# Optimization experiments

Hardware: AMD Instinct MI355X
Metric: run time of the kernel (lower is better)

Reference implementation:

```python
import jax, jax.numpy as jnp
import numpy as np

B, S, IN, H, Q, M, K = 32, 2048, 128, 256, 16, 64, 3


def setup_inputs() -> dict:
    key = jax.random.key(0)
    ks = jax.random.split(key, 12)
    rn = lambda k, shp, s=0.05: (jax.random.normal(k, shp, jnp.float32) * s)
    return {
        "input_sequence": rn(ks[0], (B, S, IN), 1.0),
        "W_ih0": rn(ks[1], (4 * H, IN)),
        "W_hh0": rn(ks[2], (4 * H, H)),
        "b_ih0": jnp.zeros((4 * H,), jnp.float32),
        "b_hh0": jnp.zeros((4 * H,), jnp.float32),
        "W_ih1": rn(ks[3], (4 * H, H)),
        "W_hh1": rn(ks[4], (4 * H, H)),
        "b_ih1": jnp.zeros((4 * H,), jnp.float32),
        "b_hh1": jnp.zeros((4 * H,), jnp.float32),
        "W_cq": rn(ks[5], (Q, H)),
        "b_cq": jnp.zeros((Q,), jnp.float32),
        "mem_keys": rn(ks[6], (M, Q), 1.0),
        "mem_vals": rn(ks[7], (M, H), 1.0),
        "W_out": rn(ks[8], (H, 2 * H)),
        "b_out": jnp.zeros((H,), jnp.float32),
        "classical_weight": jnp.float32(0.7),
        "quantum_weight": jnp.float32(0.3),
    }


def _lstm_layer(x, W_ih, W_hh, b_ih, b_hh):
    """PyTorch-convention LSTM layer (gate order i,f,g,o), batch_first input."""
    Bb = x.shape[0]
    Hh = W_hh.shape[1]
    # precompute the input contribution for all timesteps: [B,S,4H]
    xg = jnp.einsum('bsi,gi->bsg', x, W_ih) + b_ih + b_hh

    def step(carry, xt):
        h, c = carry
        g = xt + h @ W_hh.T  # [B,4H]
        i, f, gg, o = jnp.split(g, 4, axis=-1)
        i = jax.nn.sigmoid(i)
        f = jax.nn.sigmoid(f)
        gg = jnp.tanh(gg)
        o = jax.nn.sigmoid(o)
        c = f * c + i * gg
        h = o * jnp.tanh(c)
        return (h, c), h

    init = (jnp.zeros((Bb, Hh), x.dtype), jnp.zeros((Bb, Hh), x.dtype))
    _, hs = jax.lax.scan(step, init, jnp.swapaxes(xg, 0, 1))  # [S,B,H]
    return jnp.swapaxes(hs, 0, 1)


def _forward(input_sequence, W_ih0, W_hh0, b_ih0, b_hh0, W_ih1, W_hh1, b_ih1,
             b_hh1, W_cq, b_cq, mem_keys, mem_vals, W_out, b_out,
             classical_weight, quantum_weight):
    # classical 2-layer LSTM
    h1 = _lstm_layer(input_sequence, W_ih0, W_hh0, b_ih0, b_hh0)
    lstm_out = _lstm_layer(h1, W_ih1, W_hh1, b_ih1, b_hh1)  # [B,S,H]

    # classical_to_quantum + tanh -> per-token query [B,S,Q]
    q = jnp.tanh(jnp.einsum('bsh,qh->bsq', lstm_out, W_cq) + b_cq)

    # batched k-NN read over the quantum memory (cosine similarity, k=3)
    eps = jnp.float32(1e-8)
    qn = q / (jnp.linalg.norm(q, axis=-1, keepdims=True) + eps)
    kn = mem_keys / (jnp.linalg.norm(mem_keys, axis=-1, keepdims=True) + eps)
    sims = jnp.einsum('bsq,mq->bsm', qn, kn)          # [B,S,M]
    top_vals, top_idx = jax.lax.top_k(sims, K)        # [B,S,K]
    gathered = mem_vals[top_idx]                      # [B,S,K,H]

    # similarity-weighted average of retrieved contents
    tot = jnp.sum(top_vals, axis=-1, keepdims=True)   # [B,S,1]
    weighted = jnp.einsum('bsk,bskh->bsh', top_vals, gathered)
    enhanced = jnp.where(tot > 0, weighted / jnp.where(tot == 0, 1.0, tot), 0.0)

    # combine streams and project
    combined = jnp.concatenate(
        [classical_weight * lstm_out, quantum_weight * enhanced], axis=-1)
    out = jnp.einsum('bsc,hc->bsh', combined, W_out) + b_out  # [B,S,H]
    return out


def reference(input_sequence, W_ih0, W_hh0, b_ih0, b_hh0, W_ih1, W_hh1, b_ih1,
              b_hh1, W_cq, b_cq, mem_keys, mem_vals, W_out, b_out,
              classical_weight, quantum_weight):
    return _forward(input_sequence, W_ih0, W_hh0, b_ih0, b_hh0, W_ih1, W_hh1,
                    b_ih1, b_hh1, W_cq, b_cq, mem_keys, mem_vals, W_out, b_out,
                    classical_weight, quantum_weight)
```

## Files before the change

kernel.cpp:

```cpp
#include <hip/hip_runtime.h>
#include <cstdint>
#include <cstddef>
#include <math.h>

#define B_   32
#define S_   2048
#define IN_  128
#define H_   256
#define Q_   16
#define M_   64
#define D_   4

__device__ __forceinline__ float4 ld4(const float* p) { return *(const float4*)p; }

#define AGLD(p)    __hip_atomic_load((p),  __ATOMIC_RELAXED, __HIP_MEMORY_SCOPE_AGENT)
#define AGST(p, v) __hip_atomic_store((p), (v), __ATOMIC_RELAXED, __HIP_MEMORY_SCOPE_AGENT)

__global__ __launch_bounds__(256, 1) void lstm2(
    const float* __restrict__ x,
    const float* __restrict__ Wih0, const float* __restrict__ bih0,
    const float* __restrict__ bhh0, const float* __restrict__ Whh0,
    const float* __restrict__ Wih1, const float* __restrict__ bih1,
    const float* __restrict__ bhh1, const float* __restrict__ Whh1,
    float* __restrict__ out,
    unsigned int* __restrict__ ex)
{
  const int f = blockIdx.x;
  const int n = (f >> 3) & 7;
  const int b = (f >> 6) * 8 + (f & 7);

  const int tid  = threadIdx.x;
  const int w    = tid >> 6;
  const int l    = tid & 63;
  const int cl   = l >> 1;
  const int half = l & 1;

  __shared__ float wih1_lds[128 * 257];
  __shared__ float aring[8][256];
  __shared__ float h_sh[256];
  __shared__ float x_sh[2][IN_];
  __shared__ float g0_sh[4][32], g1_sh[4][32];

#pragma unroll
  for (int s2 = 0; s2 < 8; s2++) aring[s2][tid] = 0.0f;
  h_sh[tid] = 0.0f;

  const int grow = w * 256 + n * 32 + cl;

  float4 wf0[32], wf1[32], wi0[16];
  {
    const float* p0  = Whh0 + (size_t)grow * 256 + half * 128;
    const float* p1  = Whh1 + (size_t)grow * 256 + half * 128;
    const float* pi0 = Wih0 + (size_t)grow * IN_ + half * 64;
#pragma unroll
    for (int i = 0; i < 32; i++) { wf0[i] = ld4(p0 + 4 * i); wf1[i] = ld4(p1 + 4 * i); }
#pragma unroll
    for (int i = 0; i < 16; i++) wi0[i] = ld4(pi0 + 4 * i);
  }
  {
    const int r = tid >> 1, hs = tid & 1;
    const int growR = (r >> 5) * 256 + n * 32 + (r & 31);
    const float* src = Wih1 + (size_t)growR * 256 + hs * 128;
    float* dst = wih1_lds + r * 257 + hs * 128;
#pragma unroll
    for (int i = 0; i < 32; i++) *(float4*)(dst + 4 * i) = ld4(src + 4 * i);
  }
  const float rb0 = (half == 0) ? (bih0[grow] + bhh0[grow]) : 0.0f;
  const float rb1 = (half == 0) ? (bih1[grow] + bhh1[grow]) : 0.0f;
  const float* wih1_row = wih1_lds + (w * 32 + cl) * 257 + half * 128;

  const float* xrow = x + (size_t)b * S_ * IN_;
  float* outp = out + (size_t)b * S_ * H_;
  unsigned int* exb = ex + (size_t)b * 2048;

  if (tid < IN_) {
    x_sh[0][tid] = xrow[tid];
    x_sh[1][tid] = xrow[IN_ + tid];
  }
  float xreg = (tid < IN_) ? xrow[(size_t)2 * IN_ + tid] : 0.0f;
  float c0 = 0.0f, c1 = 0.0f;
  float xa1 = 0.0f;
  __syncthreads();

  float xa0;
  {
    const float* xb = &x_sh[0][half * 64];
    float4 s = {0, 0, 0, 0};
#pragma unroll
    for (int i = 0; i < 16; i++) {
      float4 v = *(const float4*)(xb + 4 * i);
      s.x += wi0[i].x * v.x; s.y += wi0[i].y * v.y;
      s.z += wi0[i].z * v.z; s.w += wi0[i].w * v.w;
    }
    xa0 = (s.x + s.y) + (s.z + s.w) + rb0;
  }

  bool dead = false;
  for (int t = 0; t < S_ + D_; ++t) {
    const bool doA = (t < S_);
    const int  u   = t - D_;
    const bool doH = (u >= 0);

    float g0 = 0.0f, g1 = 0.0f;
    if (doA) {
      const float* ap = &aring[(t - 1) & 7][half * 128];
      float4 s = {0, 0, 0, 0};
#pragma unroll
      for (int i = 0; i < 32; i++) {
        float4 v = *(const float4*)(ap + 4 * i);
        s.x += wf0[i].x * v.x; s.y += wf0[i].y * v.y;
        s.z += wf0[i].z * v.z; s.w += wf0[i].w * v.w;
      }
      g0 = (s.x + s.y) + (s.z + s.w) + xa0;
      g0 += __shfl_xor(g0, 1);
    }
    if (doH) {
      const float* hp = &h_sh[half * 128];
      float4 s = {0, 0, 0, 0};
#pragma unroll
      for (int i = 0; i < 32; i++) {
        float4 v = *(const float4*)(hp + 4 * i);
        s.x += wf1[i].x * v.x; s.y += wf1[i].y * v.y;
        s.z += wf1[i].z * v.z; s.w += wf1[i].w * v.w;
      }
      g1 = (s.x + s.y) + (s.z + s.w) + xa1;
      g1 += __shfl_xor(g1, 1);
    }
    if (half == 0) {
      if (doA) g0_sh[w][cl] = g0;
      if (doH) g1_sh[w][cl] = g1;
    }
    __syncthreads();

    if (tid < 32 && doA) {
      float gi = g0_sh[0][tid], gf = g0_sh[1][tid];
      float gg = g0_sh[2][tid], go = g0_sh[3][tid];
      float ig = 1.0f / (1.0f + expf(-gi));
      float fg = 1.0f / (1.0f + expf(-gf));
      float cg = tanhf(gg);
      float og = 1.0f / (1.0f + expf(-go));
      c0 = fg * c0 + ig * cg;
      float a = og * tanhf(c0);
      unsigned bits = __float_as_uint(a);
      unsigned tag  = (unsigned)(t + 1) << 16;
      const int p = t & 1, e = n * 32 + tid;
      AGST(exb + (((0 * 2 + p) * 2 + 0) << 8) + e, tag | (bits >> 16));
      AGST(exb + (((0 * 2 + p) * 2 + 1) << 8) + e, tag | (bits & 0xffffu));
    } else if (tid >= 64 && tid < 96 && doH) {
      const int j = tid - 64;
      float gi = g1_sh[0][j], gf = g1_sh[1][j];
      float gg = g1_sh[2][j], go = g1_sh[3][j];
      float ig = 1.0f / (1.0f + expf(-gi));
      float fg = 1.0f / (1.0f + expf(-gf));
      float cg = tanhf(gg);
      float og = 1.0f / (1.0f + expf(-go));
      c1 = fg * c1 + ig * cg;
      float h = og * tanhf(c1);
      outp[(size_t)u * H_ + n * 32 + j] = h;
      unsigned bits = __float_as_uint(h);
      unsigned tag  = (unsigned)(u + 1) << 16;
      const int p = u & 1, e = n * 32 + j;
      AGST(exb + (((1 * 2 + p) * 2 + 0) << 8) + e, tag | (bits >> 16));
      AGST(exb + (((1 * 2 + p) * 2 + 1) << 8) + e, tag | (bits & 0xffffu));
    }

    if (t + 1 < S_) {
      const float* xb = &x_sh[(t + 1) & 1][half * 64];
      float4 s = {0, 0, 0, 0};
#pragma unroll
      for (int i = 0; i < 16; i++) {
        float4 v = *(const float4*)(xb + 4 * i);
        s.x += wi0[i].x * v.x; s.y += wi0[i].y * v.y;
        s.z += wi0[i].z * v.z; s.w += wi0[i].w * v.w;
      }
      xa0 = (s.x + s.y) + (s.z + s.w) + rb0;
    }
    {
      const int v = t - D_ + 1;
      if (v >= 0 && v < S_) {
        const float* av = &aring[v & 7][half * 128];
        float4 s = {0, 0, 0, 0};
#pragma unroll
        for (int i = 0; i < 32; i++) {
          float4 wv = *(const float4*)(wih1_row + 4 * i);
          float4 a4 = *(const float4*)(av + 4 * i);
          s.x += wv.x * a4.x; s.y += wv.y * a4.y;
          s.z += wv.z * a4.z; s.w += wv.w * a4.w;
        }
        xa1 = (s.x + s.y) + (s.z + s.w) + rb1;
      }
    }
    float xreg_n = 0.0f;
    if (tid < IN_ && t + 2 < S_) {
      int tn = (t + 3 < S_) ? t + 3 : S_ - 1;
      xreg_n = xrow[(size_t)tn * IN_ + tid];
    }

    if (!dead && (doA || doH)) {
      const unsigned eA = (unsigned)(t + 1) & 0xffffu;
      const unsigned eH = (unsigned)(u + 1) & 0xffffu;
      const int pa = t & 1, ph = u & 1;
      unsigned int* aHi = exb + (((0 * 2 + pa) * 2 + 0) << 8) + tid;
      unsigned int* aLo = exb + (((0 * 2 + pa) * 2 + 1) << 8) + tid;
      unsigned int* hHi = exb + (((1 * 2 + ph) * 2 + 0) << 8) + tid;
      unsigned int* hLo = exb + (((1 * 2 + ph) * 2 + 1) << 8) + tid;
      unsigned a0v = 0, a1v = 0, h0v = 0, h1v = 0;
      bool needA = doA, needH = doH;
      unsigned guard = 0;
      while (true) {
        if (needA) {
          a0v = AGLD(aHi); a1v = AGLD(aLo);
          if ((a0v >> 16) == eA && (a1v >> 16) == eA) needA = false;
        }
        if (needH) {
          h0v = AGLD(hHi); h1v = AGLD(hLo);
          if ((h0v >> 16) == eH && (h1v >> 16) == eH) needH = false;
        }
        if (!needA && !needH) break;
        if (++guard >= (1u << 20)) { dead = true; break; }
      }
      if (doA) aring[t & 7][tid] = __uint_as_float((a0v << 16) | (a1v & 0xffffu));
      if (doH) h_sh[tid]         = __uint_as_float((h0v << 16) | (h1v & 0xffffu));
    }
    if (tid < IN_ && t < S_) x_sh[t & 1][tid] = xreg;
    xreg = xreg_n;
    __syncthreads();
  }
}

__global__ __launch_bounds__(256) void knn_enh(
    const float* __restrict__ lstm, const float* __restrict__ Wcq,
    const float* __restrict__ bcq, const float* __restrict__ keys,
    const float* __restrict__ vals, const float* __restrict__ qwp,
    float* __restrict__ enh)
{
  const int tid  = threadIdx.x;
  const int wave = tid >> 6, lane = tid & 63;
  const int t = blockIdx.x * 4 + wave;

  __shared__ float xsh[4][256];
  __shared__ float qsh[4][16];

  const float* xrow = lstm + (size_t)t * H_;
  float4 x4 = ld4(xrow + lane * 4);
  *(float4*)&xsh[wave][lane * 4] = x4;
  __syncthreads();

  const int j = lane & 15, seg = lane >> 4;
  const float* wrow = Wcq + j * H_ + seg * 64;
  const float* xseg = &xsh[wave][seg * 64];
  float p = 0.0f;
#pragma unroll
  for (int c = 0; c < 64; c += 4) {
    float4 w4 = ld4(wrow + c);
    p += w4.x * xseg[c] + w4.y * xseg[c + 1] + w4.z * xseg[c + 2] + w4.w * xseg[c + 3];
  }
  p += __shfl_xor(p, 16);
  p += __shfl_xor(p, 32);
  float q = tanhf(p + bcq[j]);

  float sq = q * q;
  sq += __shfl_xor(sq, 1); sq += __shfl_xor(sq, 2);
  sq += __shfl_xor(sq, 4); sq += __shfl_xor(sq, 8);
  float qn = q / (sqrtf(sq) + 1e-8f);
  if (lane < 16) qsh[wave][lane] = qn;
  __syncthreads();

  const int m = lane;
  const float* krow = keys + m * Q_;
  float kv[16]; float kn2 = 0.0f;
#pragma unroll
  for (int jj = 0; jj < 16; jj++) { kv[jj] = krow[jj]; kn2 += kv[jj] * kv[jj]; }
  float rn = 1.0f / (sqrtf(kn2) + 1e-8f);
  float sim = 0.0f;
#pragma unroll
  for (int jj = 0; jj < 16; jj++) sim += qsh[wave][jj] * kv[jj];
  sim *= rn;

  float rem = sim;
  float tv[3]; int ti[3];
#pragma unroll
  for (int k = 0; k < 3; k++) {
    float v = rem; int idx = m;
#pragma unroll
    for (int d = 1; d < 64; d <<= 1) {
      float ov = __shfl_xor(v, d);
      int   oi = __shfl_xor(idx, d);
      if (ov > v || (ov == v && oi < idx)) { v = ov; idx = oi; }
    }
    tv[k] = v; ti[k] = idx;
    if (m == idx) rem = -INFINITY;
  }
  float tot = tv[0] + tv[1] + tv[2];

  float ex = 0, ey = 0, ez = 0, ew = 0;
#pragma unroll
  for (int k = 0; k < 3; k++) {
    float4 vv = ld4(vals + (size_t)ti[k] * H_ + lane * 4);
    ex += tv[k] * vv.x; ey += tv[k] * vv.y;
    ez += tv[k] * vv.z; ew += tv[k] * vv.w;
  }
  float inv = (tot > 0.0f) ? 1.0f / tot : 0.0f;
  const float qw = qwp[0];

  float4 o;
  o.x = qw * ex * inv; o.y = qw * ey * inv;
  o.z = qw * ez * inv; o.w = qw * ew * inv;
  *(float4*)&enh[(size_t)t * H_ + lane * 4] = o;
}

__global__ __launch_bounds__(256) void gemm_cat(
    float* __restrict__ io, const float* __restrict__ A2,
    const float* __restrict__ Bw, const float* __restrict__ bias,
    const float* __restrict__ cwp)
{
  __shared__ float As[16][68];
  __shared__ float Bs[16][260];
  const int tid  = threadIdx.x;
  const int row0 = blockIdx.x * 64;
  const int tx = tid & 15, ty = tid >> 4;
  const int lr = tid >> 2;
  const int lk = (tid & 3) << 2;
  const float cw = cwp[0];

  float acc[4][16];
#pragma unroll
  for (int i = 0; i < 4; i++)
#pragma unroll
    for (int j = 0; j < 16; j++) acc[i][j] = 0.0f;

  for (int k0 = 0; k0 < 512; k0 += 16) {
    float4 av;
    if (k0 < 256) {
      av = ld4(io + (size_t)(row0 + lr) * 256 + k0 + lk);
      av.x *= cw; av.y *= cw; av.z *= cw; av.w *= cw;
    } else {
      av = ld4(A2 + (size_t)(row0 + lr) * 256 + (k0 - 256) + lk);
    }
    As[lk + 0][lr] = av.x; As[lk + 1][lr] = av.y;
    As[lk + 2][lr] = av.z; As[lk + 3][lr] = av.w;
    const float* bp = Bw + (size_t)tid * 512 + k0;
#pragma unroll
    for (int q = 0; q < 4; q++) {
      float4 b4 = ld4(bp + 4 * q);
      Bs[4 * q + 0][tid] = b4.x; Bs[4 * q + 1][tid] = b4.y;
      Bs[4 * q + 2][tid] = b4.z; Bs[4 * q + 3][tid] = b4.w;
    }
    __syncthreads();
#pragma unroll
    for (int k = 0; k < 16; k++) {
      float4 a4 = *(const float4*)&As[k][ty << 2];
      float aa[4] = {a4.x, a4.y, a4.z, a4.w};
#pragma unroll
      for (int cc = 0; cc < 4; cc++) {
        float4 b4 = *(const float4*)&Bs[k][cc * 64 + (tx << 2)];
        float bb[4] = {b4.x, b4.y, b4.z, b4.w};
#pragma unroll
        for (int i = 0; i < 4; i++)
#pragma unroll
          for (int jj = 0; jj < 4; jj++) acc[i][cc * 4 + jj] += aa[i] * bb[jj];
      }
    }
    __syncthreads();
  }

#pragma unroll
  for (int i = 0; i < 4; i++) {
#pragma unroll
    for (int cc = 0; cc < 4; cc++) {
      int c0 = cc * 64 + (tx << 2);
      float4 o;
      o.x = acc[i][cc * 4 + 0] + bias[c0 + 0];
      o.y = acc[i][cc * 4 + 1] + bias[c0 + 1];
      o.z = acc[i][cc * 4 + 2] + bias[c0 + 2];
      o.w = acc[i][cc * 4 + 3] + bias[c0 + 3];
      *(float4*)&io[(size_t)(row0 + (ty << 2) + i) * 256 + c0] = o;
    }
  }
}

extern "C" void kernel_launch(void* const* d_in, const int* in_sizes, int n_in,
                              void* d_out, int out_size, void* d_ws, size_t ws_size,
                              hipStream_t stream)
{
  const float* x    = (const float*)d_in[0];
  const float* Wih0 = (const float*)d_in[1];
  const float* Whh0 = (const float*)d_in[2];
  const float* bih0 = (const float*)d_in[3];
  const float* bhh0 = (const float*)d_in[4];
  const float* Wih1 = (const float*)d_in[5];
  const float* Whh1 = (const float*)d_in[6];
  const float* bih1 = (const float*)d_in[7];
  const float* bhh1 = (const float*)d_in[8];
  const float* Wcq  = (const float*)d_in[9];
  const float* bcq  = (const float*)d_in[10];
  const float* keys = (const float*)d_in[11];
  const float* vals = (const float*)d_in[12];
  const float* Wout = (const float*)d_in[13];
  const float* bout = (const float*)d_in[14];
  const float* cw   = (const float*)d_in[15];
  const float* qw   = (const float*)d_in[16];
  float* out = (float*)d_out;

  const size_t HE = (size_t)B_ * S_ * H_;
  if (ws_size < HE * sizeof(float)) return;
  unsigned int* ex = (unsigned int*)d_ws;
  float* enh = (float*)d_ws;

  const int MT = B_ * S_;
  dim3 blk(256);

  hipMemsetAsync(ex, 0, (size_t)32 * 2048 * sizeof(unsigned int), stream);
  lstm2<<<dim3(256), blk, 0, stream>>>(x, Wih0, bih0, bhh0, Whh0,
                                       Wih1, bih1, bhh1, Whh1, out, ex);

  knn_enh<<<dim3(MT / 4), blk, 0, stream>>>(out, Wcq, bcq, keys, vals, qw, enh);

  gemm_cat<<<dim3(MT / 64), blk, 0, stream>>>(out, enh, Wout, bout, cw);
}
```

Baseline: 15.51 ms.

## Compute all four gates per column group to remove intra-step barrier

Restructures the per-step work mapping so that each group of 8 lanes owns one hidden column and computes all four gate dot products, reducing them with xor shuffles. The gate nonlinearities and cell update are then done redundantly in every lane of the group, which eliminates the shared-memory gate staging and the mid-step __syncthreads. The hidden-state buffer becomes a double-buffered ring so the single remaining barrier is enough. The trade-off is more shuffle reductions and redundant transcendental work, plus a different LDS access pattern for the weights and activations.

```diff
diff --git a/kernel.cpp b/kernel.cpp
--- a/kernel.cpp
+++ b/kernel.cpp
@@ -29,45 +29,46 @@
   const int n = (f >> 3) & 7;
   const int b = (f >> 6) * 8 + (f & 7);
 
-  const int tid  = threadIdx.x;
-  const int w    = tid >> 6;
-  const int l    = tid & 63;
-  const int cl   = l >> 1;
-  const int half = l & 1;
-
-  __shared__ float wih1_lds[128 * 257];
+  const int tid = threadIdx.x;
+  const int w   = tid >> 6;
+  const int l   = tid & 63;
+  const int kc  = l & 7;
+  const int rg  = l >> 3;
+  const int wrg = w * 8 + rg;
+  const int col = n * 32 + wrg;
+
+  __shared__ float w1[128][257];
   __shared__ float aring[8][256];
-  __shared__ float h_sh[256];
+  __shared__ float hring[2][256];
   __shared__ float x_sh[2][IN_];
-  __shared__ float g0_sh[4][32], g1_sh[4][32];
 
 #pragma unroll
   for (int s2 = 0; s2 < 8; s2++) aring[s2][tid] = 0.0f;
-  h_sh[tid] = 0.0f;
-
-  const int grow = w * 256 + n * 32 + cl;
-
-  float4 wf0[32], wf1[32], wi0[16];
-  {
-    const float* p0  = Whh0 + (size_t)grow * 256 + half * 128;
-    const float* p1  = Whh1 + (size_t)grow * 256 + half * 128;
-    const float* pi0 = Wih0 + (size_t)grow * IN_ + half * 64;
-#pragma unroll
-    for (int i = 0; i < 32; i++) { wf0[i] = ld4(p0 + 4 * i); wf1[i] = ld4(p1 + 4 * i); }
-#pragma unroll
-    for (int i = 0; i < 16; i++) wi0[i] = ld4(pi0 + 4 * i);
-  }
-  {
-    const int r = tid >> 1, hs = tid & 1;
-    const int growR = (r >> 5) * 256 + n * 32 + (r & 31);
-    const float* src = Wih1 + (size_t)growR * 256 + hs * 128;
-    float* dst = wih1_lds + r * 257 + hs * 128;
-#pragma unroll
-    for (int i = 0; i < 32; i++) *(float4*)(dst + 4 * i) = ld4(src + 4 * i);
-  }
-  const float rb0 = (half == 0) ? (bih0[grow] + bhh0[grow]) : 0.0f;
-  const float rb1 = (half == 0) ? (bih1[grow] + bhh1[grow]) : 0.0f;
-  const float* wih1_row = wih1_lds + (w * 32 + cl) * 257 + half * 128;
+  hring[0][tid] = 0.0f;
+  hring[1][tid] = 0.0f;
+
+  float4 wf0[4][8], wf1[4][8], wi0[4][4];
+  float rb0[4], rb1[4];
+#pragma unroll
+  for (int g = 0; g < 4; g++) {
+    const int row = g * 256 + col;
+    const float* p0 = Whh0 + (size_t)row * 256 + 4 * kc;
+    const float* p1 = Whh1 + (size_t)row * 256 + 4 * kc;
+    const float* pi = Wih0 + (size_t)row * 128 + 4 * kc;
+#pragma unroll
+    for (int j = 0; j < 8; j++) {
+      wf0[g][j] = ld4(p0 + 32 * j);
+      wf1[g][j] = ld4(p1 + 32 * j);
+    }
+#pragma unroll
+    for (int j = 0; j < 4; j++) wi0[g][j] = ld4(pi + 32 * j);
+    rb0[g] = bih0[row] + bhh0[row];
+    rb1[g] = bih1[row] + bhh1[row];
+    const float* pw = Wih1 + (size_t)row * 256 + 4 * kc;
+    float* dst = &w1[g * 32 + wrg][4 * kc];
+#pragma unroll
+    for (int j = 0; j < 8; j++) *(float4*)(dst + 32 * j) = ld4(pw + 32 * j);
+  }
 
   const float* xrow = x + (size_t)b * S_ * IN_;
   float* outp = out + (size_t)b * S_ * H_;
@@ -78,21 +79,27 @@
     x_sh[1][tid] = xrow[IN_ + tid];
   }
   float xreg = (tid < IN_) ? xrow[(size_t)2 * IN_ + tid] : 0.0f;
-  float c0 = 0.0f, c1 = 0.0f;
-  float xa1 = 0.0f;
+  float cst0 = 0.0f, cst1 = 0.0f;
+  float xa0s[4], xa1s[4] = {0, 0, 0, 0};
   __syncthreads();
 
-  float xa0;
   {
-    const float* xb = &x_sh[0][half * 64];
-    float4 s = {0, 0, 0, 0};
-#pragma unroll
-    for (int i = 0; i < 16; i++) {
-      float4 v = *(const float4*)(xb + 4 * i);
-      s.x += wi0[i].x * v.x; s.y += wi0[i].y * v.y;
-      s.z += wi0[i].z * v.z; s.w += wi0[i].w * v.w;
-    }
-    xa0 = (s.x + s.y) + (s.z + s.w) + rb0;
+    const float* xb = x_sh[0];
+    float4 xv[4];
+#pragma unroll
+    for (int j = 0; j < 4; j++) xv[j] = ld4(xb + 4 * kc + 32 * j);
+#pragma unroll
+    for (int g = 0; g < 4; g++) {
+      float4 s4 = {0, 0, 0, 0};
+#pragma unroll
+      for (int j = 0; j < 4; j++) {
+        s4.x += wi0[g][j].x * xv[j].x; s4.y += wi0[g][j].y * xv[j].y;
+        s4.z += wi0[g][j].z * xv[j].z; s4.w += wi0[g][j].w * xv[j].w;
+      }
+      float s = (s4.x + s4.y) + (s4.z + s4.w);
+      s += __shfl_xor(s, 1); s += __shfl_xor(s, 2); s += __shfl_xor(s, 4);
+      xa0s[g] = s + rb0[g];
+    }
   }
 
   bool dead = false;
@@ -101,93 +108,111 @@
     const int  u   = t - D_;
     const bool doH = (u >= 0);
 
-    float g0 = 0.0f, g1 = 0.0f;
     if (doA) {
-      const float* ap = &aring[(t - 1) & 7][half * 128];
-      float4 s = {0, 0, 0, 0};
-#pragma unroll
-      for (int i = 0; i < 32; i++) {
-        float4 v = *(const float4*)(ap + 4 * i);
-        s.x += wf0[i].x * v.x; s.y += wf0[i].y * v.y;
-        s.z += wf0[i].z * v.z; s.w += wf0[i].w * v.w;
-      }
-      g0 = (s.x + s.y) + (s.z + s.w) + xa0;
-      g0 += __shfl_xor(g0, 1);
+      const float* ap = aring[(t - 1) & 7];
+      float4 av[8];
+#pragma unroll
+      for (int j = 0; j < 8; j++) av[j] = ld4(ap + 4 * kc + 32 * j);
+      float gv[4];
+#pragma unroll
+      for (int g = 0; g < 4; g++) {
+        float4 s4 = {0, 0, 0, 0};
+#pragma unroll
+        for (int j = 0; j < 8; j++) {
+          s4.x += wf0[g][j].x * av[j].x; s4.y += wf0[g][j].y * av[j].y;
+          s4.z += wf0[g][j].z * av[j].z; s4.w += wf0[g][j].w * av[j].w;
+        }
+        float s = (s4.x + s4.y) + (s4.z + s4.w);
+        s += __shfl_xor(s, 1); s += __shfl_xor(s, 2); s += __shfl_xor(s, 4);
+        gv[g] = s + xa0s[g];
+      }
+      float ig = 1.0f / (1.0f + expf(-gv[0]));
+      float fg = 1.0f / (1.0f + expf(-gv[1]));
+      float cg = tanhf(gv[2]);
+      float og = 1.0f / (1.0f + expf(-gv[3]));
+      cst0 = fg * cst0 + ig * cg;
+      float a = og * tanhf(cst0);
+      if (kc == 0) {
+        unsigned bits = __float_as_uint(a);
+        unsigned tag  = (unsigned)(t + 1) << 16;
+        const int p = t & 1;
+        AGST(exb + (((0 * 2 + p) * 2 + 0) << 8) + col, tag | (bits >> 16));
+        AGST(exb + (((0 * 2 + p) * 2 + 1) << 8) + col, tag | (bits & 0xffffu));
+      }
     }
     if (doH) {
-      const float* hp = &h_sh[half * 128];
-      float4 s = {0, 0, 0, 0};
-#pragma unroll
-      for (int i = 0; i < 32; i++) {
-        float4 v = *(const float4*)(hp + 4 * i);
-        s.x += wf1[i].x * v.x; s.y += wf1[i].y * v.y;
-        s.z += wf1[i].z * v.z; s.w += wf1[i].w * v.w;
-      }
-      g1 = (s.x + s.y) + (s.z + s.w) + xa1;
-      g1 += __shfl_xor(g1, 1);
-    }
-    if (half == 0) {
-      if (doA) g0_sh[w][cl] = g0;
-      if (doH) g1_sh[w][cl] = g1;
-    }
-    __syncthreads();
-
-    if (tid < 32 && doA) {
-      float gi = g0_sh[0][tid], gf = g0_sh[1][tid];
-      float gg = g0_sh[2][tid], go = g0_sh[3][tid];
-      float ig = 1.0f / (1.0f + expf(-gi));
-      float fg = 1.0f / (1.0f + expf(-gf));
-      float cg = tanhf(gg);
-      float og = 1.0f / (1.0f + expf(-go));
-      c0 = fg * c0 + ig * cg;
-      float a = og * tanhf(c0);
-      unsigned bits = __float_as_uint(a);
-      unsigned tag  = (unsigned)(t + 1) << 16;
-      const int p = t & 1, e = n * 32 + tid;
-      AGST(exb + (((0 * 2 + p) * 2 + 0) << 8) + e, tag | (bits >> 16));
-      AGST(exb + (((0 * 2 + p) * 2 + 1) << 8) + e, tag | (bits & 0xffffu));
-    } else if (tid >= 64 && tid < 96 && doH) {
-      const int j = tid - 64;
-      float gi = g1_sh[0][j], gf = g1_sh[1][j];
-      float gg = g1_sh[2][j], go = g1_sh[3][j];
-      float ig = 1.0f / (1.0f + expf(-gi));
-      float fg = 1.0f / (1.0f + expf(-gf));
-      float cg = tanhf(gg);
-      float og = 1.0f / (1.0f + expf(-go));
-      c1 = fg * c1 + ig * cg;
-      float h = og * tanhf(c1);
-      outp[(size_t)u * H_ + n * 32 + j] = h;
-      unsigned bits = __float_as_uint(h);
-      unsigned tag  = (unsigned)(u + 1) << 16;
-      const int p = u & 1, e = n * 32 + j;
-      AGST(exb + (((1 * 2 + p) * 2 + 0) << 8) + e, tag | (bits >> 16));
-      AGST(exb + (((1 * 2 + p) * 2 + 1) << 8) + e, tag | (bits & 0xffffu));
+      const float* hp = hring[(t - 1) & 1];
+      float4 hv[8];
+#pragma unroll
+      for (int j = 0; j < 8; j++) hv[j] = ld4(hp + 4 * kc + 32 * j);
+      float gv[4];
+#pragma unroll
+      for (int g = 0; g < 4; g++) {
+        float4 s4 = {0, 0, 0, 0};
+#pragma unroll
+        for (int j = 0; j < 8; j++) {
+          s4.x += wf1[g][j].x * hv[j].x; s4.y += wf1[g][j].y * hv[j].y;
+          s4.z += wf1[g][j].z * hv[j].z; s4.w += wf1[g][j].w * hv[j].w;
+        }
+        float s = (s4.x + s4.y) + (s4.z + s4.w);
+        s += __shfl_xor(s, 1); s += __shfl_xor(s, 2); s += __shfl_xor(s, 4);
+        gv[g] = s + xa1s[g];
+      }
+      float ig = 1.0f / (1.0f + expf(-gv[0]));
+      float fg = 1.0f / (1.0f + expf(-gv[1]));
+      float cg = tanhf(gv[2]);
+      float og = 1.0f / (1.0f + expf(-gv[3]));
+      cst1 = fg * cst1 + ig * cg;
+      float h = og * tanhf(cst1);
+      if (kc == 0) {
+        outp[(size_t)u * H_ + col] = h;
+        unsigned bits = __float_as_uint(h);
+        unsigned tag  = (unsigned)(u + 1) << 16;
+        const int p = u & 1;
+        AGST(exb + (((1 * 2 + p) * 2 + 0) << 8) + col, tag | (bits >> 16));
+        AGST(exb + (((1 * 2 + p) * 2 + 1) << 8) + col, tag | (bits & 0xffffu));
+      }
     }
 
     if (t + 1 < S_) {
-      const float* xb = &x_sh[(t + 1) & 1][half * 64];
-      float4 s = {0, 0, 0, 0};
-#pragma unroll
-      for (int i = 0; i < 16; i++) {
-        float4 v = *(const float4*)(xb + 4 * i);
-        s.x += wi0[i].x * v.x; s.y += wi0[i].y * v.y;
-        s.z += wi0[i].z * v.z; s.w += wi0[i].w * v.w;
-      }
-      xa0 = (s.x + s.y) + (s.z + s.w) + rb0;
+      const float* xb = x_sh[(t + 1) & 1];
+      float4 xv[4];
+#pragma unroll
+      for (int j = 0; j < 4; j++) xv[j] = ld4(xb + 4 * kc + 32 * j);
+#pragma unroll
+      for (int g = 0; g < 4; g++) {
+        float4 s4 = {0, 0, 0, 0};
+#pragma unroll
+        for (int j = 0; j < 4; j++) {
+          s4.x += wi0[g][j].x * xv[j].x; s4.y += wi0[g][j].y * xv[j].y;
+          s4.z += wi0[g][j].z * xv[j].z; s4.w += wi0[g][j].w * xv[j].w;
+        }
+        float s = (s4.x + s4.y) + (s4.z + s4.w);
+        s += __shfl_xor(s, 1); s += __shfl_xor(s, 2); s += __shfl_xor(s, 4);
+        xa0s[g] = s + rb0[g];
+      }
     }
     {
       const int v = t - D_ + 1;
       if (v >= 0 && v < S_) {
-        const float* av = &aring[v & 7][half * 128];
-        float4 s = {0, 0, 0, 0};
-#pragma unroll
-        for (int i = 0; i < 32; i++) {
-          float4 wv = *(const float4*)(wih1_row + 4 * i);
-          float4 a4 = *(const float4*)(av + 4 * i);
-          s.x += wv.x * a4.x; s.y += wv.y * a4.y;
-          s.z += wv.z * a4.z; s.w += wv.w * a4.w;
-        }
-        xa1 = (s.x + s.y) + (s.z + s.w) + rb1;
+        const float* avp = aring[v & 7];
+        float4 av[8];
+#pragma unroll
+        for (int j = 0; j < 8; j++) av[j] = ld4(avp + 4 * kc + 32 * j);
+#pragma unroll
+        for (int g = 0; g < 4; g++) {
+          const float* wr = &w1[g * 32 + wrg][4 * kc];
+          float4 s4 = {0, 0, 0, 0};
+#pragma unroll
+          for (int j = 0; j < 8; j++) {
+            float4 wv = ld4(wr + 32 * j);
+            s4.x += wv.x * av[j].x; s4.y += wv.y * av[j].y;
+            s4.z += wv.z * av[j].z; s4.w += wv.w * av[j].w;
+          }
+          float s = (s4.x + s4.y) + (s4.z + s4.w);
+          s += __shfl_xor(s, 1); s += __shfl_xor(s, 2); s += __shfl_xor(s, 4);
+          xa1s[g] = s + rb1[g];
+        }
       }
     }
     float xreg_n = 0.0f;
@@ -220,7 +245,7 @@
         if (++guard >= (1u << 20)) { dead = true; break; }
       }
       if (doA) aring[t & 7][tid] = __uint_as_float((a0v << 16) | (a1v & 0xffffu));
-      if (doH) h_sh[tid]         = __uint_as_float((h0v << 16) | (h1v & 0xffffu));
+      if (doH) hring[t & 1][tid] = __uint_as_float((h0v << 16) | (h1v & 0xffffu));
     }
     if (tid < IN_ && t < S_) x_sh[t & 1][tid] = xreg;
     xreg = xreg_n;
```

After: 14.47 ms. 1.07x faster.
